# Kernel optimization log

Hardware: AMD Instinct MI355X
Metric: run time of the kernel (lower is better)

Reference implementation:

```python
import jax, jax.numpy as jnp
import numpy as np

N_HEAD = 16


def setup_inputs() -> dict:
    key = jax.random.key(0)
    k1, k2, k3 = jax.random.split(key, 3)
    B, T, N = 4, 2048, 1024
    x = jax.random.normal(k1, (B, T, N), dtype=jnp.float32)
    W_attn = jax.random.normal(k2, (N, 3 * N), dtype=jnp.float32) * (1.0 / np.sqrt(N))
    b_attn = jnp.zeros((3 * N,), dtype=jnp.float32)
    W_proj = jax.random.normal(k3, (N, N), dtype=jnp.float32) * (1.0 / np.sqrt(N))
    b_proj = jnp.zeros((N,), dtype=jnp.float32)
    return {"x": x, "W_attn": W_attn, "b_attn": b_attn, "W_proj": W_proj, "b_proj": b_proj}


def reference(x, W_attn, b_attn, W_proj, b_proj):
    B, T, N = x.shape
    H = N_HEAD
    Dh = N // H
    qkv = x @ W_attn + b_attn                      # [B, T, 3N]
    q, k, v = jnp.split(qkv, 3, axis=2)
    # [B, H, T, Dh]
    q = q.reshape(B, T, H, Dh).transpose(0, 2, 1, 3)
    k = k.reshape(B, T, H, Dh).transpose(0, 2, 1, 3)
    v = v.reshape(B, T, H, Dh).transpose(0, 2, 1, 3)
    att = jnp.einsum('bhqd,bhkd->bhqk', q, k) / (Dh ** 0.5)
    mask = jnp.tril(jnp.ones((T, T), dtype=bool))
    att = jnp.where(mask[None, None], att, jnp.finfo(x.dtype).min)
    att = jax.nn.softmax(att, axis=-1)
    y = jnp.einsum('bhqk,bhkd->bhqd', att, v)      # [B, H, T, Dh]
    y = y.transpose(0, 2, 1, 3).reshape(B, T, N)
    return y @ W_proj + b_proj
```

## Files before the change

### kernel.cpp

```cpp
#include <hip/hip_runtime.h>
#include <hip/hip_bf16.h>


typedef __attribute__((ext_vector_type(8))) short short8;
typedef __attribute__((ext_vector_type(4))) float f32x4;
typedef __attribute__((ext_vector_type(16))) float f32x16;

#define MFMA16(a, b, c) __builtin_amdgcn_mfma_f32_16x16x32_bf16((a), (b), (c), 0, 0, 0)
#define MFMA32(a, b, c) __builtin_amdgcn_mfma_f32_32x32x16_bf16((a), (b), (c), 0, 0, 0)

#if defined(__has_builtin)
#if __has_builtin(__builtin_amdgcn_exp2f)
#define EXP2(x) __builtin_amdgcn_exp2f(x)
#endif
#endif
#ifndef EXP2
#define EXP2(x) exp2f(x)
#endif

__device__ __forceinline__ void gload_lds16(const void* g, void* l) {
  __builtin_amdgcn_global_load_lds(
      (const __attribute__((address_space(1))) unsigned int*)g,
      (__attribute__((address_space(3))) unsigned int*)l, 16, 0, 0);
}

__device__ __forceinline__ unsigned pack_bf16x2(float lo, float hi) {
  unsigned ulo = __float_as_uint(lo) + 0x8000u;
  unsigned uhi = __float_as_uint(hi) + 0x8000u;
  return __builtin_amdgcn_perm(uhi, ulo, 0x07060302u);
}

__device__ __forceinline__ unsigned short bf16u(float f) {
  return (unsigned short)((__float_as_uint(f) + 0x8000u) >> 16);
}

__global__ void prep_kernel(const float* __restrict__ x, unsigned* __restrict__ Xb,
                            const float* __restrict__ Wa, __hip_bfloat16* __restrict__ WaT,
                            const float* __restrict__ Wp, __hip_bfloat16* __restrict__ WpT) {
  __shared__ float tile[32][33];
  const int tid = threadIdx.x;
  int blk = blockIdx.x;
  if (blk >= 4096) {
    int i = (blk - 4096) * 256 + tid;
    float4 v = ((const float4*)x)[i];
    uint2 o;
    o.x = pack_bf16x2(v.x, v.y);
    o.y = pack_bf16x2(v.z, v.w);
    ((uint2*)Xb)[i] = o;
    return;
  }
  const float* src;
  __hip_bfloat16* dst;
  int R, C, bx, by;
  if (blk < 3072) {
    src = Wa; dst = WaT; R = 1024; C = 3072; bx = blk % 96; by = blk / 96;
  } else {
    blk -= 3072;
    src = Wp; dst = WpT; R = 1024; C = 1024; bx = blk & 31; by = blk >> 5;
  }
  const int tx = tid & 31, ty = tid >> 5;
  const int c0 = bx * 32, r0 = by * 32;
#pragma unroll
  for (int i = 0; i < 32; i += 8)
    tile[ty + i][tx] = src[(long)(r0 + ty + i) * C + c0 + tx];
  __syncthreads();
#pragma unroll
  for (int i = 0; i < 32; i += 8)
    dst[(long)(c0 + ty + i) * R + r0 + tx] = __float2bfloat16(tile[tx][ty + i]);
}

template <int EPI>
__global__ __launch_bounds__(256, 2) void gemm_bt(
    const __hip_bfloat16* __restrict__ A, const __hip_bfloat16* __restrict__ Bt,
    const float* __restrict__ bias, void* o0, void* o1, void* o2, int N, int K) {
  __shared__ alignas(16) char smem[34816];
  short8 (*As)[8] = (short8(*)[8])smem;
  short8 (*Bs)[8] = (short8(*)[8])(smem + 16384);
  unsigned short (*C16)[136] = (unsigned short(*)[136])smem;
  float (*C32)[132] = (float(*)[132])smem;

  const int tid = threadIdx.x;
  const int lane = tid & 63, w = tid >> 6;
  const int l15 = lane & 15, quad = lane >> 4;
  const int wm = (w >> 1) * 64, wn = (w & 1) * 64;
  const int rowBase = blockIdx.y * 128;
  const int colBase = blockIdx.x * 128;
  const int sr8 = lane >> 3;
  const int scc = (lane & 7) ^ sr8;

  f32x4 acc[4][4];
#pragma unroll
  for (int mi = 0; mi < 4; ++mi)
#pragma unroll
    for (int ni = 0; ni < 4; ++ni)
      acc[mi][ni] = {0.f, 0.f, 0.f, 0.f};

  for (int k0 = 0; k0 < K; k0 += 64) {
    __syncthreads();
#pragma unroll
    for (int p = 0; p < 4; ++p) {
      const int rb = p * 32 + w * 8;
      const int row = rb + sr8;
      gload_lds16(A + (rowBase + row) * K + k0 + scc * 8, &As[rb][0]);
      gload_lds16(Bt + (colBase + row) * K + k0 + scc * 8, &Bs[rb][0]);
    }
    __syncthreads();
#pragma unroll
    for (int kc = 0; kc < 2; ++kc) {
      short8 af[4], bf[4];
#pragma unroll
      for (int mi = 0; mi < 4; ++mi) {
        int row = wm + mi * 16 + l15;
        af[mi] = As[row][(kc * 4 + quad) ^ (row & 7)];
      }
#pragma unroll
      for (int ni = 0; ni < 4; ++ni) {
        int row = wn + ni * 16 + l15;
        bf[ni] = Bs[row][(kc * 4 + quad) ^ (row & 7)];
      }
#pragma unroll
      for (int mi = 0; mi < 4; ++mi)
#pragma unroll
        for (int ni = 0; ni < 4; ++ni)
          acc[mi][ni] = MFMA16(af[mi], bf[ni], acc[mi][ni]);
    }
  }

  float bcol[4];
#pragma unroll
  for (int ni = 0; ni < 4; ++ni) bcol[ni] = bias[colBase + wn + ni * 16 + l15];

  if (EPI == 0) {
    const int which = colBase >> 10;
    const int b = rowBase >> 11;
    const int tt0 = rowBase & 2047;
    const int n1base = colBase & 1023;
    const float osc = (which == 0) ? 0.180336880111f : 1.0f;
    __syncthreads();
    if (which != 2) {
#pragma unroll
      for (int mi = 0; mi < 4; ++mi)
#pragma unroll
        for (int ni = 0; ni < 4; ++ni)
#pragma unroll
          for (int r = 0; r < 4; ++r)
            C16[wm + mi * 16 + quad * 4 + r][wn + ni * 16 + l15] =
                bf16u((acc[mi][ni][r] + bcol[ni]) * osc);
    } else {
#pragma unroll
      for (int mi = 0; mi < 4; ++mi)
#pragma unroll
        for (int ni = 0; ni < 4; ++ni)
#pragma unroll
          for (int r = 0; r < 4; ++r)
            C16[wn + ni * 16 + l15][wm + mi * 16 + quad * 4 + r] =
                bf16u(acc[mi][ni][r] + bcol[ni]);
    }
    __syncthreads();
    unsigned short* o = (unsigned short*)(which == 0 ? o0 : which == 1 ? o1 : o2);
    if (which != 2) {
#pragma unroll
      for (int j = 0; j < 8; ++j) {
        int flat = j * 256 + tid;
        int trow = flat >> 4, ch = flat & 15;
        int h = (n1base + ((ch & 8) << 3)) >> 6;
        long addr = ((long)((b * 16 + h) * 2048 + tt0 + trow)) * 64 + (ch & 7) * 8;
        *(short8*)&o[addr] = *(const short8*)&C16[trow][ch * 8];
      }
    } else {
#pragma unroll
      for (int j = 0; j < 8; ++j) {
        int flat = j * 256 + tid;
        int dcol = flat >> 4, ch = flat & 15;
        int h = (n1base + (dcol & 64)) >> 6;
        long addr = ((long)((b * 16 + h) * 64 + (dcol & 63))) * 2048 + tt0 + ch * 8;
        *(short8*)&o[addr] = *(const short8*)&C16[dcol][ch * 8];
      }
    }
  } else {
    float* out = (float*)o0;
    for (int p = 0; p < 2; ++p) {
      __syncthreads();
      if ((w >> 1) == p) {
#pragma unroll
        for (int mi = 0; mi < 4; ++mi)
#pragma unroll
          for (int ni = 0; ni < 4; ++ni)
#pragma unroll
            for (int r = 0; r < 4; ++r)
              C32[mi * 16 + quad * 4 + r][wn + ni * 16 + l15] =
                  acc[mi][ni][r] + bcol[ni];
      }
      __syncthreads();
#pragma unroll
      for (int j = 0; j < 8; ++j) {
        int flat = j * 256 + tid;
        int row = flat >> 5, ch = flat & 31;
        float4 v4 = *(const float4*)&C32[row][ch * 4];
        *(float4*)&out[(long)(rowBase + p * 64 + row) * N + colBase + ch * 4] = v4;
      }
    }
  }
}

__global__ __launch_bounds__(256, 3) void attn_kernel(
    const __hip_bfloat16* __restrict__ Q, const __hip_bfloat16* __restrict__ K,
    const __hip_bfloat16* __restrict__ Vt, __hip_bfloat16* __restrict__ Y, int T) {
  __shared__ short8 Ks[3][64][8];
  __shared__ short8 Vs[3][64][8];
  const int tid = threadIdx.x;
  const int w = tid >> 6, lane = tid & 63;
  const int c31 = lane & 31, half = lane >> 5;
  const int rsw = c31 & 7;
  const int idx = blockIdx.x;
  const int bh = idx & 63;
  const int b = bh >> 4, h = bh & 15;
  const int qsel = idx >> 6;
  const int qq = qsel >> 2, qp = qsel & 3;
  const int jt = (qq == 0) ? 15 - qp : (qq == 1) ? 8 + qp : (qq == 2) ? 4 + qp : 3 - qp;

  const int qrow0 = jt * 128 + w * 32;
  const __hip_bfloat16* Qp = Q + (long)bh * T * 64;
  const __hip_bfloat16* Kp = K + (long)bh * T * 64;
  const __hip_bfloat16* Vp = Vt + (long)bh * 64 * T;

  const int sr8 = lane >> 3;
  const int scc = (lane & 7) ^ sr8;

  short8 qf[4];
#pragma unroll
  for (int s = 0; s < 4; ++s)
    qf[s] = *(const short8*)(Qp + (qrow0 + c31) * 64 + s * 16 + half * 8);

  f32x16 czero;
#pragma unroll
  for (int i = 0; i < 16; ++i) czero[i] = 0.f;
  f32x16 oacc[2];
#pragma unroll
  for (int g = 0; g < 2; ++g) oacc[g] = czero;
  float lsum = 0.f;
  const int myq = qrow0 + c31;
  const int nkt = 2 * jt + 2;
  const int my_nkt = 2 * jt + 1 + (w >> 1);
  const int my_diag = my_nkt - 1;

#define STAGE_ATTN(buf, kbase)                                                 \
  do {                                                                         \
    const int rb_ = w * 16;                                                    \
    gload_lds16(Kp + ((kbase) + rb_ + sr8) * 64 + scc * 8, &Ks[buf][rb_][0]);  \
    gload_lds16(Kp + ((kbase) + rb_ + 8 + sr8) * 64 + scc * 8,                 \
                &Ks[buf][rb_ + 8][0]);                                         \
    gload_lds16(Vp + (long)(rb_ + sr8) * T + (kbase) + scc * 8,                \
                &Vs[buf][rb_][0]);                                             \
    gload_lds16(Vp + (long)(rb_ + 8 + sr8) * T + (kbase) + scc * 8,            \
                &Vs[buf][rb_ + 8][0]);                                         \
  } while (0)

  STAGE_ATTN(0, 0);
  STAGE_ATTN(1, 64);
  int bcur = 0;

  for (int kt = 0; kt < nkt; ++kt) {
    if (kt < nkt - 1)
      asm volatile("s_waitcnt vmcnt(4)" ::: "memory");
    else
      asm volatile("s_waitcnt vmcnt(0)" ::: "memory");
    __builtin_amdgcn_s_barrier();
    __builtin_amdgcn_sched_barrier(0);

    if (kt + 2 < nkt) {
      const int bs = (bcur >= 1) ? bcur - 1 : 2;
      STAGE_ATTN(bs, (kt + 2) * 64);
    }

    if (kt < my_nkt) {
      const int kb = kt * 64;
      short8 pb[4];
#pragma unroll
      for (int g = 0; g < 2; ++g) {
        short8 af[4];
#pragma unroll
        for (int s = 0; s < 4; ++s)
          af[s] = Ks[bcur][g * 32 + c31][(s * 2 + half) ^ rsw];
        __builtin_amdgcn_s_setprio(1);
        f32x16 z = MFMA32(af[0], qf[0], czero);
#pragma unroll
        for (int s = 1; s < 4; ++s) z = MFMA32(af[s], qf[s], z);
        __builtin_amdgcn_s_setprio(0);
        if (kt == my_diag) {
#pragma unroll
          for (int r = 0; r < 16; ++r) {
            int key = kb + g * 32 + (r & 3) + 8 * (r >> 2) + 4 * half;
            if (key > myq) z[r] = -INFINITY;
          }
        }
        unsigned pk[8];
#pragma unroll
        for (int i = 0; i < 8; ++i) {
          float p0 = EXP2(z[2 * i]);
          float p1 = EXP2(z[2 * i + 1]);
          lsum += p0 + p1;
          pk[i] = pack_bf16x2(p0, p1);
        }
#pragma unroll
        for (int s = 0; s < 2; ++s) {
          auto r0 = __builtin_amdgcn_permlane32_swap(pk[4 * s + 0], pk[4 * s + 2],
                                                     false, false);
          auto r1 = __builtin_amdgcn_permlane32_swap(pk[4 * s + 1], pk[4 * s + 3],
                                                     false, false);
          union { unsigned u[4]; short8 s8; } cv;
          cv.u[0] = r0[0]; cv.u[1] = r1[0]; cv.u[2] = r0[1]; cv.u[3] = r1[1];
          pb[g * 2 + s] = cv.s8;
        }
      }
#pragma unroll
      for (int dg = 0; dg < 2; ++dg) {
        short8 vf[4];
#pragma unroll
        for (int S = 0; S < 4; ++S)
          vf[S] = Vs[bcur][dg * 32 + c31][(S * 2 + half) ^ rsw];
        __builtin_amdgcn_s_setprio(1);
#pragma unroll
        for (int S = 0; S < 4; ++S)
          oacc[dg] = MFMA32(vf[S], pb[S], oacc[dg]);
        __builtin_amdgcn_s_setprio(0);
      }
    }
    bcur = (bcur == 2) ? 0 : bcur + 1;
  }

  lsum += __shfl_xor(lsum, 32);

  const float inv = 1.0f / lsum;
  unsigned short* Yu = (unsigned short*)Y;
  const long rowoff = ((long)(b * 2048 + qrow0 + c31)) * 1024 + h * 64;
#pragma unroll
  for (int dg = 0; dg < 2; ++dg)
#pragma unroll
    for (int rg = 0; rg < 4; ++rg) {
      uint2 o;
      o.x = pack_bf16x2(oacc[dg][rg * 4 + 0] * inv, oacc[dg][rg * 4 + 1] * inv);
      o.y = pack_bf16x2(oacc[dg][rg * 4 + 2] * inv, oacc[dg][rg * 4 + 3] * inv);
      *(uint2*)&Yu[rowoff + dg * 32 + half * 4 + rg * 8] = o;
    }
}

extern "C" void kernel_launch(void* const* d_in, const int* in_sizes, int n_in,
                              void* d_out, int out_size, void* d_ws, size_t ws_size,
                              hipStream_t stream) {
  const float* x  = (const float*)d_in[0];
  const float* Wa = (const float*)d_in[1];
  const float* ba = (const float*)d_in[2];
  const float* Wp = (const float*)d_in[3];
  const float* bp = (const float*)d_in[4];
  float* out = (float*)d_out;

  char* ws = (char*)d_ws;
  __hip_bfloat16* Xb  = (__hip_bfloat16*)(ws);
  __hip_bfloat16* WaT = (__hip_bfloat16*)(ws + 16777216);
  __hip_bfloat16* WpT = (__hip_bfloat16*)(ws + 23068672);
  __hip_bfloat16* Qb  = (__hip_bfloat16*)(ws + 25165824);
  __hip_bfloat16* Kb  = (__hip_bfloat16*)(ws + 41943040);
  __hip_bfloat16* Vtb = (__hip_bfloat16*)(ws + 58720256);
  __hip_bfloat16* Yb  = (__hip_bfloat16*)(ws + 75497472);
  if (ws_size < 92274688) return;

  prep_kernel<<<12288, 256, 0, stream>>>(x, (unsigned*)Xb, Wa, WaT, Wp, WpT);
  gemm_bt<0><<<dim3(24, 64), 256, 0, stream>>>(Xb, WaT, ba, Qb, Kb, Vtb, 3072, 1024);
  attn_kernel<<<dim3(1024), dim3(256), 0, stream>>>(Qb, Kb, Vtb, Yb, 2048);
  gemm_bt<1><<<dim3(8, 64), 256, 0, stream>>>(Yb, WpT, bp, out, nullptr, nullptr, 1024, 1024);
}
```

Baseline: 222.7 us.

## Shrink attention key tile to 32 and raise occupancy to 4 blocks per CU

The attention kernel now walks keys in 32-row tiles instead of 64, halving the LDS staging buffers and remapping the V transpose staging layout so one load per thread fills each tile. Launch bounds rise from 3 to 4 blocks per SM, and causal work per wave is balanced at finer granularity because each wave stops one 32-key tile apart instead of two waves sharing a 64-key stop. In exchange there are twice as many loop iterations and barriers, with fewer MFMAs per barrier to hide load latency, and the higher occupancy target may tighten register limits.

```diff
diff --git a/kernel.cpp b/kernel.cpp
--- a/kernel.cpp
+++ b/kernel.cpp
@@ -203,11 +203,11 @@
   }
 }
 
-__global__ __launch_bounds__(256, 3) void attn_kernel(
+__global__ __launch_bounds__(256, 4) void attn_kernel(
     const __hip_bfloat16* __restrict__ Q, const __hip_bfloat16* __restrict__ K,
     const __hip_bfloat16* __restrict__ Vt, __hip_bfloat16* __restrict__ Y, int T) {
-  __shared__ short8 Ks[3][64][8];
-  __shared__ short8 Vs[3][64][8];
+  __shared__ short8 Ks[3][32][8];
+  __shared__ short8 Vs[3][32][8];
   const int tid = threadIdx.x;
   const int w = tid >> 6, lane = tid & 63;
   const int c31 = lane & 31, half = lane >> 5;
@@ -225,7 +225,10 @@
   const __hip_bfloat16* Vp = Vt + (long)bh * 64 * T;
 
   const int sr8 = lane >> 3;
-  const int scc = (lane & 7) ^ sr8;
+  const int srow = w * 8 + sr8;
+  const int scc = (lane & 7) ^ (srow & 7);
+  const int vrow = srow + ((scc >> 2) << 5);
+  const int vkoff = (scc & 3) * 8;
 
   short8 qf[4];
 #pragma unroll
@@ -240,29 +243,23 @@
   for (int g = 0; g < 2; ++g) oacc[g] = czero;
   float lsum = 0.f;
   const int myq = qrow0 + c31;
-  const int nkt = 2 * jt + 2;
-  const int my_nkt = 2 * jt + 1 + (w >> 1);
+  const int nkt = 4 * jt + 4;
+  const int my_nkt = 4 * jt + w + 1;
   const int my_diag = my_nkt - 1;
 
-#define STAGE_ATTN(buf, kbase)                                                 \
-  do {                                                                         \
-    const int rb_ = w * 16;                                                    \
-    gload_lds16(Kp + ((kbase) + rb_ + sr8) * 64 + scc * 8, &Ks[buf][rb_][0]);  \
-    gload_lds16(Kp + ((kbase) + rb_ + 8 + sr8) * 64 + scc * 8,                 \
-                &Ks[buf][rb_ + 8][0]);                                         \
-    gload_lds16(Vp + (long)(rb_ + sr8) * T + (kbase) + scc * 8,                \
-                &Vs[buf][rb_][0]);                                             \
-    gload_lds16(Vp + (long)(rb_ + 8 + sr8) * T + (kbase) + scc * 8,            \
-                &Vs[buf][rb_ + 8][0]);                                         \
+#define STAGE_ATTN(buf, kbase)                                             \
+  do {                                                                     \
+    gload_lds16(Kp + ((kbase) + srow) * 64 + scc * 8, &Ks[buf][w * 8][0]); \
+    gload_lds16(Vp + (long)vrow * T + (kbase) + vkoff, &Vs[buf][w * 8][0]);\
   } while (0)
 
   STAGE_ATTN(0, 0);
-  STAGE_ATTN(1, 64);
+  STAGE_ATTN(1, 32);
   int bcur = 0;
 
   for (int kt = 0; kt < nkt; ++kt) {
     if (kt < nkt - 1)
-      asm volatile("s_waitcnt vmcnt(4)" ::: "memory");
+      asm volatile("s_waitcnt vmcnt(2)" ::: "memory");
     else
       asm volatile("s_waitcnt vmcnt(0)" ::: "memory");
     __builtin_amdgcn_s_barrier();
@@ -270,61 +267,59 @@
 
     if (kt + 2 < nkt) {
       const int bs = (bcur >= 1) ? bcur - 1 : 2;
-      STAGE_ATTN(bs, (kt + 2) * 64);
+      STAGE_ATTN(bs, (kt + 2) * 32);
     }
 
     if (kt < my_nkt) {
-      const int kb = kt * 64;
-      short8 pb[4];
-#pragma unroll
-      for (int g = 0; g < 2; ++g) {
-        short8 af[4];
-#pragma unroll
-        for (int s = 0; s < 4; ++s)
-          af[s] = Ks[bcur][g * 32 + c31][(s * 2 + half) ^ rsw];
-        __builtin_amdgcn_s_setprio(1);
-        f32x16 z = MFMA32(af[0], qf[0], czero);
-#pragma unroll
-        for (int s = 1; s < 4; ++s) z = MFMA32(af[s], qf[s], z);
-        __builtin_amdgcn_s_setprio(0);
-        if (kt == my_diag) {
-#pragma unroll
-          for (int r = 0; r < 16; ++r) {
-            int key = kb + g * 32 + (r & 3) + 8 * (r >> 2) + 4 * half;
-            if (key > myq) z[r] = -INFINITY;
-          }
+      const int kb = kt * 32;
+      short8 af[4];
+#pragma unroll
+      for (int s = 0; s < 4; ++s)
+        af[s] = Ks[bcur][c31][(s * 2 + half) ^ rsw];
+      __builtin_amdgcn_s_setprio(1);
+      f32x16 z = MFMA32(af[0], qf[0], czero);
+#pragma unroll
+      for (int s = 1; s < 4; ++s) z = MFMA32(af[s], qf[s], z);
+      __builtin_amdgcn_s_setprio(0);
+      if (kt == my_diag) {
+#pragma unroll
+        for (int r = 0; r < 16; ++r) {
+          int key = kb + (r & 3) + 8 * (r >> 2) + 4 * half;
+          if (key > myq) z[r] = -INFINITY;
         }
-        unsigned pk[8];
-#pragma unroll
-        for (int i = 0; i < 8; ++i) {
-          float p0 = EXP2(z[2 * i]);
-          float p1 = EXP2(z[2 * i + 1]);
-          lsum += p0 + p1;
-          pk[i] = pack_bf16x2(p0, p1);
-        }
-#pragma unroll
-        for (int s = 0; s < 2; ++s) {
-          auto r0 = __builtin_amdgcn_permlane32_swap(pk[4 * s + 0], pk[4 * s + 2],
-                                                     false, false);
-          auto r1 = __builtin_amdgcn_permlane32_swap(pk[4 * s + 1], pk[4 * s + 3],
-                                                     false, false);
-          union { unsigned u[4]; short8 s8; } cv;
-          cv.u[0] = r0[0]; cv.u[1] = r1[0]; cv.u[2] = r0[1]; cv.u[3] = r1[1];
-          pb[g * 2 + s] = cv.s8;
-        }
-      }
-#pragma unroll
-      for (int dg = 0; dg < 2; ++dg) {
-        short8 vf[4];
-#pragma unroll
-        for (int S = 0; S < 4; ++S)
-          vf[S] = Vs[bcur][dg * 32 + c31][(S * 2 + half) ^ rsw];
-        __builtin_amdgcn_s_setprio(1);
-#pragma unroll
-        for (int S = 0; S < 4; ++S)
-          oacc[dg] = MFMA32(vf[S], pb[S], oacc[dg]);
-        __builtin_amdgcn_s_setprio(0);
-      }
+      }
+      unsigned pk[8];
+#pragma unroll
+      for (int i = 0; i < 8; ++i) {
+        float p0 = EXP2(z[2 * i]);
+        float p1 = EXP2(z[2 * i + 1]);
+        lsum += p0 + p1;
+        pk[i] = pack_bf16x2(p0, p1);
+      }
+      short8 pb[2];
+#pragma unroll
+      for (int s = 0; s < 2; ++s) {
+        auto r0 = __builtin_amdgcn_permlane32_swap(pk[4 * s + 0], pk[4 * s + 2],
+                                                   false, false);
+        auto r1 = __builtin_amdgcn_permlane32_swap(pk[4 * s + 1], pk[4 * s + 3],
+                                                   false, false);
+        union { unsigned u[4]; short8 s8; } cv;
+        cv.u[0] = r0[0]; cv.u[1] = r1[0]; cv.u[2] = r0[1]; cv.u[3] = r1[1];
+        pb[s] = cv.s8;
+      }
+      short8 vf[2][2];
+#pragma unroll
+      for (int dg = 0; dg < 2; ++dg)
+#pragma unroll
+        for (int S = 0; S < 2; ++S)
+          vf[dg][S] = Vs[bcur][c31][(dg * 4 + S * 2 + half) ^ rsw];
+      __builtin_amdgcn_s_setprio(1);
+#pragma unroll
+      for (int dg = 0; dg < 2; ++dg)
+#pragma unroll
+        for (int S = 0; S < 2; ++S)
+          oacc[dg] = MFMA32(vf[dg][S], pb[S], oacc[dg]);
+      __builtin_amdgcn_s_setprio(0);
     }
     bcur = (bcur == 2) ? 0 : bcur + 1;
   }
```

Result: no change. 226.5 us (+1.7%).

## Fuse prep, QKV GEMM, attention and projection into persistent mega-kernel with grid barriers

Applied to the files above, without the earlier changes.

Replaces the four separate launches (convert/transpose, QKV GEMM, attention, output projection) with one persistent kernel of 512 blocks. The phases are separated by atomic-counter grid barriers, and each phase uses grid-stride loops over its work items. Attention pairs a long and a short causal query tile per block to balance the load. This removes inter-kernel launch gaps and tail effects, but caps occupancy at 2 blocks per CU (attention previously ran 3), needs every block co-resident, and keeps the barrier counter in the last 64 bytes of the output buffer, which the final GEMM overwrites.

```diff
diff --git a/kernel.cpp b/kernel.cpp
--- a/kernel.cpp
+++ b/kernel.cpp
@@ -18,6 +18,8 @@
 #define EXP2(x) exp2f(x)
 #endif
 
+#define NBLK 512
+
 __device__ __forceinline__ void gload_lds16(const void* g, void* l) {
   __builtin_amdgcn_global_load_lds(
       (const __attribute__((address_space(1))) unsigned int*)g,
@@ -34,57 +36,33 @@
   return (unsigned short)((__float_as_uint(f) + 0x8000u) >> 16);
 }
 
-__global__ void prep_kernel(const float* __restrict__ x, unsigned* __restrict__ Xb,
-                            const float* __restrict__ Wa, __hip_bfloat16* __restrict__ WaT,
-                            const float* __restrict__ Wp, __hip_bfloat16* __restrict__ WpT) {
-  __shared__ float tile[32][33];
-  const int tid = threadIdx.x;
-  int blk = blockIdx.x;
-  if (blk >= 4096) {
-    int i = (blk - 4096) * 256 + tid;
-    float4 v = ((const float4*)x)[i];
-    uint2 o;
-    o.x = pack_bf16x2(v.x, v.y);
-    o.y = pack_bf16x2(v.z, v.w);
-    ((uint2*)Xb)[i] = o;
-    return;
-  }
-  const float* src;
-  __hip_bfloat16* dst;
-  int R, C, bx, by;
-  if (blk < 3072) {
-    src = Wa; dst = WaT; R = 1024; C = 3072; bx = blk % 96; by = blk / 96;
-  } else {
-    blk -= 3072;
-    src = Wp; dst = WpT; R = 1024; C = 1024; bx = blk & 31; by = blk >> 5;
-  }
-  const int tx = tid & 31, ty = tid >> 5;
-  const int c0 = bx * 32, r0 = by * 32;
-#pragma unroll
-  for (int i = 0; i < 32; i += 8)
-    tile[ty + i][tx] = src[(long)(r0 + ty + i) * C + c0 + tx];
+__device__ __forceinline__ void gridbar(unsigned* cnt, unsigned target) {
   __syncthreads();
-#pragma unroll
-  for (int i = 0; i < 32; i += 8)
-    dst[(long)(c0 + ty + i) * R + r0 + tx] = __float2bfloat16(tile[tx][ty + i]);
+  if (threadIdx.x == 0) {
+    __threadfence();
+    __hip_atomic_fetch_add(cnt, 1u, __ATOMIC_ACQ_REL, __HIP_MEMORY_SCOPE_AGENT);
+    while (__hip_atomic_load(cnt, __ATOMIC_ACQUIRE, __HIP_MEMORY_SCOPE_AGENT) < target)
+      __builtin_amdgcn_s_sleep(8);
+    __threadfence();
+  }
+  __syncthreads();
 }
 
 template <int EPI>
-__global__ __launch_bounds__(256, 2) void gemm_bt(
-    const __hip_bfloat16* __restrict__ A, const __hip_bfloat16* __restrict__ Bt,
-    const float* __restrict__ bias, void* o0, void* o1, void* o2, int N, int K) {
-  __shared__ alignas(16) char smem[34816];
+__device__ __forceinline__ void gemm_body(
+    char* smem, const __hip_bfloat16* __restrict__ A,
+    const __hip_bfloat16* __restrict__ Bt, const float* __restrict__ bias,
+    void* o0, void* o1, void* o2, int N, int K, int colb, int rowb, int tid) {
   short8 (*As)[8] = (short8(*)[8])smem;
   short8 (*Bs)[8] = (short8(*)[8])(smem + 16384);
   unsigned short (*C16)[136] = (unsigned short(*)[136])smem;
   float (*C32)[132] = (float(*)[132])smem;
 
-  const int tid = threadIdx.x;
   const int lane = tid & 63, w = tid >> 6;
   const int l15 = lane & 15, quad = lane >> 4;
   const int wm = (w >> 1) * 64, wn = (w & 1) * 64;
-  const int rowBase = blockIdx.y * 128;
-  const int colBase = blockIdx.x * 128;
+  const int rowBase = rowb * 128;
+  const int colBase = colb * 128;
   const int sr8 = lane >> 3;
   const int scc = (lane & 7) ^ sr8;
 
@@ -203,21 +181,16 @@
   }
 }
 
-__global__ __launch_bounds__(256, 3) void attn_kernel(
-    const __hip_bfloat16* __restrict__ Q, const __hip_bfloat16* __restrict__ K,
-    const __hip_bfloat16* __restrict__ Vt, __hip_bfloat16* __restrict__ Y, int T) {
-  __shared__ short8 Ks[3][64][8];
-  __shared__ short8 Vs[3][64][8];
-  const int tid = threadIdx.x;
+__device__ __forceinline__ void attn_body(
+    char* smem, const __hip_bfloat16* __restrict__ Q,
+    const __hip_bfloat16* __restrict__ K, const __hip_bfloat16* __restrict__ Vt,
+    __hip_bfloat16* __restrict__ Y, int T, int jt, int bh, int tid) {
+  short8 (*Ks)[64][8] = (short8(*)[64][8])smem;
+  short8 (*Vs)[64][8] = (short8(*)[64][8])(smem + 24576);
   const int w = tid >> 6, lane = tid & 63;
   const int c31 = lane & 31, half = lane >> 5;
   const int rsw = c31 & 7;
-  const int idx = blockIdx.x;
-  const int bh = idx & 63;
   const int b = bh >> 4, h = bh & 15;
-  const int qsel = idx >> 6;
-  const int qq = qsel >> 2, qp = qsel & 3;
-  const int jt = (qq == 0) ? 15 - qp : (qq == 1) ? 8 + qp : (qq == 2) ? 4 + qp : 3 - qp;
 
   const int qrow0 = jt * 128 + w * 32;
   const __hip_bfloat16* Qp = Q + (long)bh * T * 64;
@@ -256,6 +229,7 @@
                 &Vs[buf][rb_ + 8][0]);                                         \
   } while (0)
 
+  __syncthreads();
   STAGE_ATTN(0, 0);
   STAGE_ATTN(1, 64);
   int bcur = 0;
@@ -328,6 +302,7 @@
     }
     bcur = (bcur == 2) ? 0 : bcur + 1;
   }
+#undef STAGE_ATTN
 
   lsum += __shfl_xor(lsum, 32);
 
@@ -343,6 +318,66 @@
       o.y = pack_bf16x2(oacc[dg][rg * 4 + 2] * inv, oacc[dg][rg * 4 + 3] * inv);
       *(uint2*)&Yu[rowoff + dg * 32 + half * 4 + rg * 8] = o;
     }
+}
+
+__global__ __launch_bounds__(256, 2) void mega(
+    const float* __restrict__ x, const float* __restrict__ Wa,
+    const float* __restrict__ ba, const float* __restrict__ Wp,
+    const float* __restrict__ bp, __hip_bfloat16* Xb, __hip_bfloat16* WaT,
+    __hip_bfloat16* WpT, __hip_bfloat16* Qb, __hip_bfloat16* Kb,
+    __hip_bfloat16* Vtb, __hip_bfloat16* Yb, float* out, unsigned* cnt) {
+  __shared__ alignas(16) char smem[49152];
+  const int tid = threadIdx.x;
+  const int bid = blockIdx.x;
+
+  {
+    float (*tile)[33] = (float(*)[33])smem;
+    for (int vb = bid; vb < 12288; vb += NBLK) {
+      if (vb >= 4096) {
+        int i = (vb - 4096) * 256 + tid;
+        float4 v = ((const float4*)x)[i];
+        uint2 o;
+        o.x = pack_bf16x2(v.x, v.y);
+        o.y = pack_bf16x2(v.z, v.w);
+        ((uint2*)Xb)[i] = o;
+      } else {
+        const float* src;
+        __hip_bfloat16* dst;
+        int R, C, bx, by, blk = vb;
+        if (blk < 3072) {
+          src = Wa; dst = WaT; R = 1024; C = 3072; bx = blk % 96; by = blk / 96;
+        } else {
+          blk -= 3072;
+          src = Wp; dst = WpT; R = 1024; C = 1024; bx = blk & 31; by = blk >> 5;
+        }
+        const int tx = tid & 31, ty = tid >> 5;
+        const int c0 = bx * 32, r0 = by * 32;
+        __syncthreads();
+#pragma unroll
+        for (int i = 0; i < 32; i += 8)
+          tile[ty + i][tx] = src[(long)(r0 + ty + i) * C + c0 + tx];
+        __syncthreads();
+#pragma unroll
+        for (int i = 0; i < 32; i += 8)
+          dst[(long)(c0 + ty + i) * R + r0 + tx] = __float2bfloat16(tile[tx][ty + i]);
+      }
+    }
+  }
+  gridbar(cnt, NBLK);
+
+  for (int vb = bid; vb < 1536; vb += NBLK)
+    gemm_body<0>(smem, Xb, WaT, ba, Qb, Kb, Vtb, 3072, 1024, vb % 24, vb / 24, tid);
+  gridbar(cnt, 2 * NBLK);
+
+  {
+    const int f = bid >> 6, bh = bid & 63;
+    attn_body(smem, Qb, Kb, Vtb, Yb, 2048, 15 - f, bh, tid);
+    attn_body(smem, Qb, Kb, Vtb, Yb, 2048, f, bh, tid);
+  }
+  gridbar(cnt, 3 * NBLK);
+
+  gemm_body<1>(smem, Yb, WpT, bp, out, nullptr, nullptr, 1024, 1024,
+               bid & 7, bid >> 3, tid);
 }
 
 extern "C" void kernel_launch(void* const* d_in, const int* in_sizes, int n_in,
@@ -365,8 +400,9 @@
   __hip_bfloat16* Yb  = (__hip_bfloat16*)(ws + 75497472);
   if (ws_size < 92274688) return;
 
-  prep_kernel<<<12288, 256, 0, stream>>>(x, (unsigned*)Xb, Wa, WaT, Wp, WpT);
-  gemm_bt<0><<<dim3(24, 64), 256, 0, stream>>>(Xb, WaT, ba, Qb, Kb, Vtb, 3072, 1024);
-  attn_kernel<<<dim3(1024), dim3(256), 0, stream>>>(Qb, Kb, Vtb, Yb, 2048);
-  gemm_bt<1><<<dim3(8, 64), 256, 0, stream>>>(Yb, WpT, bp, out, nullptr, nullptr, 1024, 1024);
-}
+  unsigned* cnt = (unsigned*)((char*)d_out + 33554432 - 64);
+  hipMemsetAsync(cnt, 0, 64, stream);
+
+  mega<<<dim3(NBLK), dim3(256), 0, stream>>>(
+      x, Wa, ba, Wp, bp, Xb, WaT, WpT, Qb, Kb, Vtb, Yb, out, cnt);
+}
```

New measurement: 469.7 us. 2.11x slower.
